# Kernel optimization log

Measured on AMD Instinct MI355X. Metric: run time of the kernel, lower is better.

## Reference

```python
import jax, jax.numpy as jnp
import numpy as np

B, T, D, H = 4, 1024, 512, 8
DK = D // H
P = 2 * T - 1  # relative position length


def rel_shift(x):
    # x: (b, h, t, 2t-1) -> (b, h, t, t), Transformer-XL relative shift
    b, h, t, p = x.shape
    x = jnp.pad(x, ((0, 0), (0, 0), (0, 0), (1, 0)))  # (b,h,t,p+1)
    x = x.reshape(b, h, p + 1, t)[:, :, 1:, :].reshape(b, h, t, p)
    return x[..., :t]


def setup_inputs() -> dict:
    key = jax.random.key(0)
    ks = jax.random.split(key, 16)
    s = 0.02
    return {
        "q": jax.random.normal(ks[0], (B, T, D), jnp.float32),
        "k": jax.random.normal(ks[1], (B, T, D), jnp.float32),
        "v": jax.random.normal(ks[2], (B, T, D), jnp.float32),
        "pos_emb": jax.random.normal(ks[3], (1, P, D), jnp.float32),
        "Wq": jax.random.normal(ks[4], (D, D), jnp.float32) * s,
        "bq": jnp.zeros((D,), jnp.float32),
        "Wk": jax.random.normal(ks[5], (D, D), jnp.float32) * s,
        "bk": jnp.zeros((D,), jnp.float32),
        "Wv": jax.random.normal(ks[6], (D, D), jnp.float32) * s,
        "bv": jnp.zeros((D,), jnp.float32),
        "Wp": jax.random.normal(ks[7], (D, D), jnp.float32) * s,
        "pos_bias_u": jax.random.normal(ks[8], (H, DK), jnp.float32) * s,
        "pos_bias_v": jax.random.normal(ks[9], (H, DK), jnp.float32) * s,
        "Wo": jax.random.normal(ks[10], (D, D), jnp.float32) * s,
        "bo": jnp.zeros((D,), jnp.float32),
    }


def reference(q, k, v, pos_emb, Wq, bq, Wk, bk, Wv, bv, Wp,
              pos_bias_u, pos_bias_v, Wo, bo):
    b, t, d = q.shape
    # QKV projections, split heads -> (b, t, h, dk)
    qh = (q @ Wq.T + bq).reshape(b, t, H, DK)
    kh = (k @ Wk.T + bk).reshape(b, t, H, DK)
    vh = (v @ Wv.T + bv).reshape(b, t, H, DK)
    # positional projection (no bias): (1, P, h, dk)
    ph = (pos_emb @ Wp.T).reshape(pos_emb.shape[1], H, DK)
    # content term: (q + u) . k
    q_u = qh + pos_bias_u  # (b,t,h,dk)
    matrix_ac = jnp.einsum("bqhd,bkhd->bhqk", q_u, kh)
    # position term: (q + v) . p, then relative shift
    q_v = qh + pos_bias_v
    matrix_bd = jnp.einsum("bqhd,phd->bhqp", q_v, ph)
    matrix_bd = rel_shift(matrix_bd)  # (b,h,t,t)
    scores = (matrix_ac + matrix_bd) / jnp.sqrt(jnp.float32(DK))
    attn = jax.nn.softmax(scores, axis=-1)
    out = jnp.einsum("bhqk,bkhd->bqhd", attn, vh).reshape(b, t, d)
    return out @ Wo.T + bo
```

## Files before the change

kernel.cpp:

```cpp
#include <hip/hip_runtime.h>
#include <math.h>

typedef unsigned short u16;
typedef _Float16 f16;
typedef __attribute__((ext_vector_type(8))) _Float16 f16x8;
typedef __attribute__((ext_vector_type(4))) float f32x4;

#define B_  4
#define T_  1024
#define D_  512
#define H_  8
#define DK_ 64
#define P_  2047

#define MFMAH(a, b, c) __builtin_amdgcn_mfma_f32_16x16x32_f16(a, b, c, 0, 0, 0)

__device__ __forceinline__ u16 f2hbits(float x) {
    union { f16 h; u16 u; } cv; cv.h = (f16)x; return cv.u;
}

__device__ __forceinline__ void gload_lds16(const u16* g, u16* l) {
    __builtin_amdgcn_global_load_lds(
        (const __attribute__((address_space(1))) void*)g,
        (__attribute__((address_space(3))) void*)l, 16, 0, 0);
}

__device__ __forceinline__ int swz8(int row, int colbase) {
    return row * 64 + (((colbase >> 3) ^ (row & 7)) << 3);
}

__global__ __launch_bounds__(256)
void conv_all(const float* __restrict__ q, const float* __restrict__ k,
              const float* __restrict__ v, const float* __restrict__ pe,
              const float* __restrict__ wq, const float* __restrict__ wk,
              const float* __restrict__ wv, const float* __restrict__ wp,
              const float* __restrict__ wo,
              u16* qs, u16* ks, u16* vs, u16* pes,
              u16* wqs, u16* wks, u16* wvs, u16* wps, u16* wos)
{
    const int NQ = 524288;
    const int NPE = 262016;
    const int NW = 65536;
    const int TOT = 3 * NQ + NPE + 5 * NW;
    for (int i = blockIdx.x * 256 + threadIdx.x; i < TOT; i += gridDim.x * 256) {
        const float* src; u16* dst; int off;
        int j = i;
        if (j < NQ)              { src = q;  dst = qs;  off = j; }
        else if ((j -= NQ) < NQ) { src = k;  dst = ks;  off = j; }
        else if ((j -= NQ) < NQ) { src = v;  dst = vs;  off = j; }
        else if ((j -= NQ) < NPE){ src = pe; dst = pes; off = j; }
        else if ((j -= NPE) < NW){ src = wq; dst = wqs; off = j; }
        else if ((j -= NW) < NW) { src = wk; dst = wks; off = j; }
        else if ((j -= NW) < NW) { src = wv; dst = wvs; off = j; }
        else if ((j -= NW) < NW) { src = wp; dst = wps; off = j; }
        else                     { j -= NW; src = wo; dst = wos; off = j; }
        float4 x = *(const float4*)(src + (size_t)off * 4);
        union { f16 h[4]; uint2 u2; } cv;
        cv.h[0] = (f16)x.x; cv.h[1] = (f16)x.y;
        cv.h[2] = (f16)x.z; cv.h[3] = (f16)x.w;
        *(uint2*)(dst + (size_t)off * 4) = cv.u2;
    }
}

__device__ __forceinline__ void gemm_core(
    const u16* __restrict__ A, const u16* __restrict__ Bw,
    int bm, int bn, int M, f32x4 (&acc)[4][4],
    u16 (&sA)[2][128][64], u16 (&sB)[2][128][64])
{
    const int tid = threadIdx.x;
    const int ln = tid & 63, w = tid >> 6;
    const int arow = ln & 15, kseg = ln >> 4;
    const int wr = w >> 1, wc = w & 1;

    auto stage = [&](int k0, int buf) {
        #pragma unroll
        for (int it = 0; it < 4; ++it) {
            int ch = it * 256 + tid;
            int r = ch >> 3, j = ch & 7;
            int rm = bm + r; if (rm > M - 1) rm = M - 1;
            gload_lds16(A + (size_t)rm * 512 + k0 + ((j ^ (r & 7)) << 3),
                        &sA[buf][0][0] + ch * 8);
        }
        #pragma unroll
        for (int it = 0; it < 4; ++it) {
            int ch = it * 256 + tid;
            int r = ch >> 3, j = ch & 7;
            gload_lds16(Bw + (size_t)(bn + r) * 512 + k0 + ((j ^ (r & 7)) << 3),
                        &sB[buf][0][0] + ch * 8);
        }
    };

    stage(0, 0);
    for (int t = 0; t < 8; ++t) {
        const int cur = t & 1;
        if (t < 7) {
            stage((t + 1) * 64, cur ^ 1);
            asm volatile("s_waitcnt vmcnt(8)" ::: "memory");
        } else {
            asm volatile("s_waitcnt vmcnt(0)" ::: "memory");
        }
        __builtin_amdgcn_sched_barrier(0);
        __builtin_amdgcn_s_barrier();

        f16x8 af[4][2], bf[4][2];
        #pragma unroll
        for (int mi = 0; mi < 4; ++mi) {
            int row = wr * 64 + mi * 16 + arow;
            #pragma unroll
            for (int kc = 0; kc < 2; ++kc)
                af[mi][kc] = *(const f16x8*)
                    (&sA[cur][row][0] + ((((kc << 2) | kseg) ^ (row & 7)) << 3));
        }
        #pragma unroll
        for (int nj = 0; nj < 4; ++nj) {
            int row = wc * 64 + nj * 16 + arow;
            #pragma unroll
            for (int kc = 0; kc < 2; ++kc)
                bf[nj][kc] = *(const f16x8*)
                    (&sB[cur][row][0] + ((((kc << 2) | kseg) ^ (row & 7)) << 3));
        }
        __builtin_amdgcn_s_setprio(1);
        #pragma unroll
        for (int mi = 0; mi < 4; ++mi)
            #pragma unroll
            for (int nj = 0; nj < 4; ++nj)
                #pragma unroll
                for (int kc = 0; kc < 2; ++kc)
                    acc[mi][nj] = MFMAH(af[mi][kc], bf[nj][kc], acc[mi][nj]);
        __builtin_amdgcn_s_setprio(0);

        asm volatile("" ::: "memory");
        __builtin_amdgcn_s_barrier();
        asm volatile("" ::: "memory");
    }
}

__global__ __launch_bounds__(256, 2)
void gemm_qkvp(const u16* __restrict__ qs, const u16* __restrict__ ks,
               const u16* __restrict__ vs, const u16* __restrict__ pes,
               const u16* __restrict__ wqs, const u16* __restrict__ wks,
               const u16* __restrict__ wvs, const u16* __restrict__ wps,
               const float* __restrict__ bq, const float* __restrict__ bk,
               const float* __restrict__ bv,
               const float* __restrict__ pbu, const float* __restrict__ pbv,
               u16* __restrict__ qub, u16* __restrict__ qvb,
               u16* __restrict__ kh, u16* __restrict__ vt, u16* __restrict__ ph)
{
    __shared__ u16 sA[2][128][64];
    __shared__ u16 sB[2][128][64];

    const int by = blockIdx.y;
    const u16 *A, *Bw; const float* bias;
    int seg, bm, M, Tn;
    if (by < 32)      { seg=0; bm=by*128;       A=qs;  Bw=wqs; bias=bq;      M=4096; Tn=T_; }
    else if (by < 64) { seg=1; bm=(by-32)*128;  A=ks;  Bw=wks; bias=bk;      M=4096; Tn=T_; }
    else if (by < 96) { seg=2; bm=(by-64)*128;  A=vs;  Bw=wvs; bias=bv;      M=4096; Tn=T_; }
    else              { seg=3; bm=(by-96)*128;  A=pes; Bw=wps; bias=nullptr; M=P_;   Tn=P_; }
    const int bn = blockIdx.x * 128;

    f32x4 acc[4][4] = {};
    gemm_core(A, Bw, bm, bn, M, acc, sA, sB);

    const int tid = threadIdx.x;
    const int ln = tid & 63, w = tid >> 6;
    const int arow = ln & 15, kseg = ln >> 4;
    const int wr = w >> 1, wc = w & 1;

    float bv0[4];
    #pragma unroll
    for (int nj = 0; nj < 4; ++nj)
        bv0[nj] = bias ? bias[bn + wc * 64 + nj * 16 + arow] : 0.f;

    #pragma unroll
    for (int mi = 0; mi < 4; ++mi)
        #pragma unroll
        for (int r = 0; r < 4; ++r) {
            int m = bm + wr * 64 + mi * 16 + kseg * 4 + r;
            if (m >= M) continue;
            #pragma unroll
            for (int nj = 0; nj < 4; ++nj) {
                int n = bn + wc * 64 + nj * 16 + arow;
                float val = acc[mi][nj][r] + bv0[nj];
                if (seg == 0) {
                    int bb = m >> 10, t = m & 1023;
                    int hh = n >> 6, d = n & 63;
                    size_t off = ((size_t)(bb * H_ + hh) * T_ + t) * 64 + d;
                    qub[off] = f2hbits((val + pbu[hh * 64 + d]) * 0.125f);
                    qvb[off] = f2hbits((val + pbv[hh * 64 + d]) * 0.125f);
                } else if (seg == 2) {
                    int bb = m >> 10, t = m & 1023;
                    int hh = n >> 6, d = n & 63;
                    vt[((size_t)(bb * H_ + hh) * 64 + d) * T_ + t] = f2hbits(val);
                } else {
                    int bb = (Tn == T_) ? (m >> 10) : 0;
                    int t = m - bb * Tn;
                    int hh = n >> 6, d = n & 63;
                    size_t off = ((size_t)(bb * H_ + hh) * Tn + t) * 64 + d;
                    if (seg == 1) kh[off] = f2hbits(val);
                    else          ph[off] = f2hbits(val);
                }
            }
        }
}

__global__ __launch_bounds__(256, 2)
void gemm_out(const u16* __restrict__ A, const u16* __restrict__ Bw,
              const float* __restrict__ bias, float* __restrict__ C)
{
    __shared__ u16 sA[2][128][64];
    __shared__ u16 sB[2][128][64];
    const int bn = blockIdx.x * 128;
    const int bm = blockIdx.y * 128;
    f32x4 acc[4][4] = {};
    gemm_core(A, Bw, bm, bn, 4096, acc, sA, sB);

    const int tid = threadIdx.x;
    const int ln = tid & 63, w = tid >> 6;
    const int arow = ln & 15, kseg = ln >> 4;
    const int wr = w >> 1, wc = w & 1;
    #pragma unroll
    for (int mi = 0; mi < 4; ++mi)
        #pragma unroll
        for (int r = 0; r < 4; ++r) {
            int m = bm + wr * 64 + mi * 16 + kseg * 4 + r;
            #pragma unroll
            for (int nj = 0; nj < 4; ++nj) {
                int n = bn + wc * 64 + nj * 16 + arow;
                C[(size_t)m * 512 + n] = acc[mi][nj][r] + bias[n];
            }
        }
}

__global__ __launch_bounds__(256, 2)
void relattn_mfma(const u16* __restrict__ qub, const u16* __restrict__ qvb,
                  const u16* __restrict__ kh, const u16* __restrict__ vt,
                  const u16* __restrict__ ph,
                  u16* __restrict__ ao)
{
    __shared__ u16 s_k[3][64][64];
    __shared__ u16 s_p[3][64][64];
    __shared__ u16 s_pp[4][16][64];

    const int tid = threadIdx.x;
    const int ln  = tid & 63;
    const int w   = tid >> 6;
    const int arow = ln & 15;
    const int kseg = ln >> 4;

    const int lg = ((blockIdx.x & 7) << 6) | (blockIdx.x >> 3);
    const int qt = lg & 15, h = (lg >> 4) & 7, b = lg >> 7;
    const int q0 = qt * 64;

    const size_t kvbase = (size_t)(b * H_ + h) * T_ * 64;
    const size_t vtbase = (size_t)(b * H_ + h) * 64 * T_;
    const size_t pbase  = (size_t)h * P_ * 64;
    const int jb0 = 960 - q0;

    f16x8 qu[2], qv[2];
    {
        const u16* qb = qub + kvbase + (size_t)(q0 + w * 16 + arow) * 64;
        const u16* vb = qvb + kvbase + (size_t)(q0 + w * 16 + arow) * 64;
        #pragma unroll
        for (int c = 0; c < 2; ++c) {
            qu[c] = *(const f16x8*)(qb + c * 32 + kseg * 8);
            qv[c] = *(const f16x8*)(vb + c * 32 + kseg * 8);
        }
    }

    f32x4 o_[4] = {};
    float l_run[4] = {};

    auto stage_k = [&](int kt, int slot) {
        #pragma unroll
        for (int it = 0; it < 2; ++it) {
            int idx = tid + it * 256;
            int r = idx >> 3, ch = idx & 7;
            const u16* src = kh + kvbase + (size_t)(kt * 64 + r) * 64 + ((ch ^ (r & 7)) << 3);
            gload_lds16(src, &s_k[slot][0][0] + idx * 8);
        }
    };
    auto stage_p = [&](int c, int slot) {
        #pragma unroll
        for (int it = 0; it < 2; ++it) {
            int idx = tid + it * 256;
            int r = idx >> 3, ch = idx & 7;
            int j = jb0 + c * 64 + r; if (j > P_ - 1) j = P_ - 1;
            const u16* src = ph + pbase + (size_t)j * 64 + ((ch ^ (r & 7)) << 3);
            gload_lds16(src, &s_p[slot][0][0] + idx * 8);
        }
    };
    auto bd_chunk = [&](int slot, f32x4* out) {
        #pragma unroll
        for (int nb = 0; nb < 4; ++nb) {
            int pr = nb * 16 + arow;
            f16x8 b0 = *(const f16x8*)(&s_p[slot][0][0] + swz8(pr, kseg * 8));
            f16x8 b1 = *(const f16x8*)(&s_p[slot][0][0] + swz8(pr, 32 + kseg * 8));
            out[nb] = MFMAH(qv[0], b0, out[nb]);
            out[nb] = MFMAH(qv[1], b1, out[nb]);
        }
    };

    stage_k(0, 0); stage_k(1, 1);
    stage_p(0, 0); stage_p(1, 1); stage_p(2, 2);
    __syncthreads();
    f32x4 carry[4] = {};
    bd_chunk(0, carry);
    asm volatile("" ::: "memory");
    __builtin_amdgcn_s_barrier();
    asm volatile("" ::: "memory");

    int ks = 0;
    for (int t = 0; t < 16; ++t) {
        const int k0 = t * 64;
        const int pr = (ks + 1 > 2) ? 0 : ks + 1;
        const int kw = (ks + 2 > 2) ? ks - 1 : ks + 2;

        f16x8 vfr[4][2];
        #pragma unroll
        for (int nt = 0; nt < 4; ++nt) {
            const u16* vp = vt + vtbase + (size_t)(nt * 16 + arow) * T_ + k0 + kseg * 8;
            vfr[nt][0] = *(const f16x8*)vp;
            vfr[nt][1] = *(const f16x8*)(vp + 32);
        }

        if (t < 14) { stage_k(t + 2, kw); stage_p(t + 3, ks); }

        __builtin_amdgcn_s_setprio(1);
        f32x4 ac[4] = {};
        #pragma unroll
        for (int nt = 0; nt < 4; ++nt) {
            int kr = nt * 16 + arow;
            f16x8 b0 = *(const f16x8*)(&s_k[ks][0][0] + swz8(kr, kseg * 8));
            f16x8 b1 = *(const f16x8*)(&s_k[ks][0][0] + swz8(kr, 32 + kseg * 8));
            ac[nt] = MFMAH(qu[0], b0, ac[nt]);
            ac[nt] = MFMAH(qu[1], b1, ac[nt]);
        }
        f32x4 bdn[4] = {};
        bd_chunk(pr, bdn);
        __builtin_amdgcn_s_setprio(0);

        float win[5][4];
        #pragma unroll
        for (int r = 0; r < 4; ++r) {
            if (w == 0)      { win[0][r]=carry[3][r]; win[1][r]=bdn[0][r];   win[2][r]=bdn[1][r];   win[3][r]=bdn[2][r];   win[4][r]=bdn[3][r]; }
            else if (w == 1) { win[0][r]=carry[2][r]; win[1][r]=carry[3][r]; win[2][r]=bdn[0][r];   win[3][r]=bdn[1][r];   win[4][r]=bdn[2][r]; }
            else if (w == 2) { win[0][r]=carry[1][r]; win[1][r]=carry[2][r]; win[2][r]=carry[3][r]; win[3][r]=bdn[0][r];   win[4][r]=bdn[1][r]; }
            else             { win[0][r]=carry[0][r]; win[1][r]=carry[1][r]; win[2][r]=carry[2][r]; win[3][r]=carry[3][r]; win[4][r]=bdn[0][r]; }
        }

        #pragma unroll
        for (int r = 0; r < 4; ++r) {
            int sl  = 15 - (kseg << 2) - r;
            int src = (ln & 48) | ((arow + sl) & 15);
            bool hi = (arow < sl);
            int r16 = kseg * 4 + r;
            #pragma unroll
            for (int nt = 0; nt < 4; ++nt) {
                float sel = hi ? win[nt + 1][r] : win[nt][r];
                float pm = __shfl(sel, src, 64);
                float pv = __expf(ac[nt][r] + pm);
                l_run[r] += pv;
                int kl = nt * 16 + arow;
                s_pp[w][r16][(((kl >> 3) ^ (r16 & 7)) << 3) | (kl & 7)] = f2hbits(pv);
            }
        }
        asm volatile("s_waitcnt lgkmcnt(0)" ::: "memory");
        __builtin_amdgcn_sched_barrier(0);

        f16x8 pa0 = *(const f16x8*)(&s_pp[w][arow][0] + ((kseg ^ (arow & 7)) << 3));
        f16x8 pa1 = *(const f16x8*)(&s_pp[w][arow][0] + (((4 + kseg) ^ (arow & 7)) << 3));
        __builtin_amdgcn_s_setprio(1);
        #pragma unroll
        for (int nt = 0; nt < 4; ++nt) {
            o_[nt] = MFMAH(pa0, vfr[nt][0], o_[nt]);
            o_[nt] = MFMAH(pa1, vfr[nt][1], o_[nt]);
        }
        __builtin_amdgcn_s_setprio(0);

        #pragma unroll
        for (int nb = 0; nb < 4; ++nb) carry[nb] = bdn[nb];

        asm volatile("" ::: "memory");
        __builtin_amdgcn_s_barrier();
        asm volatile("" ::: "memory");
        ks = pr;
    }

    #pragma unroll
    for (int r = 0; r < 4; ++r) {
        float l = l_run[r];
        l += __shfl_xor(l, 1); l += __shfl_xor(l, 2);
        l += __shfl_xor(l, 4); l += __shfl_xor(l, 8);
        l_run[r] = 1.f / l;
    }
    #pragma unroll
    for (int nt = 0; nt < 4; ++nt)
        #pragma unroll
        for (int r = 0; r < 4; ++r) {
            int qrow = q0 + w * 16 + kseg * 4 + r;
            size_t off = ((size_t)(b * T_ + qrow)) * D_ + h * DK_ + nt * 16 + arow;
            ao[off] = f2hbits(o_[nt][r] * l_run[r]);
        }
}

extern "C" void kernel_launch(void* const* d_in, const int* in_sizes, int n_in,
                              void* d_out, int out_size, void* d_ws, size_t ws_size,
                              hipStream_t stream)
{
    const float* q   = (const float*)d_in[0];
    const float* k   = (const float*)d_in[1];
    const float* v   = (const float*)d_in[2];
    const float* pe  = (const float*)d_in[3];
    const float* Wq  = (const float*)d_in[4];
    const float* bq  = (const float*)d_in[5];
    const float* Wk  = (const float*)d_in[6];
    const float* bk  = (const float*)d_in[7];
    const float* Wv  = (const float*)d_in[8];
    const float* bv  = (const float*)d_in[9];
    const float* Wp  = (const float*)d_in[10];
    const float* pbu = (const float*)d_in[11];
    const float* pbv = (const float*)d_in[12];
    const float* Wo  = (const float*)d_in[13];
    const float* bo  = (const float*)d_in[14];
    float* out = (float*)d_out;

    char* ws = (char*)d_ws;
    const size_t MB = 1024 * 1024;
    const size_t HMB = 512 * 1024;
    u16* qs  = (u16*)(ws);
    u16* ks  = (u16*)(ws + 4 * MB);
    u16* vs  = (u16*)(ws + 8 * MB);
    u16* pes = (u16*)(ws + 12 * MB);
    u16* wqs = (u16*)(ws + 17 * MB);
    u16* wks = (u16*)(ws + 17 * MB + HMB);
    u16* wvs = (u16*)(ws + 18 * MB);
    u16* wps = (u16*)(ws + 18 * MB + HMB);
    u16* wos = (u16*)(ws + 19 * MB);
    u16* qub = (u16*)(ws + 20 * MB);
    u16* qvb = (u16*)(ws + 24 * MB);
    u16* kh  = (u16*)(ws + 28 * MB);
    u16* vt  = (u16*)(ws + 32 * MB);
    u16* ph  = (u16*)(ws + 36 * MB);
    u16* ao  = (u16*)(ws + 38 * MB + HMB);

    dim3 blk(256);
    conv_all<<<dim3(2048), blk, 0, stream>>>(q, k, v, pe, Wq, Wk, Wv, Wp, Wo,
        qs, ks, vs, pes, wqs, wks, wvs, wps, wos);

    gemm_qkvp<<<dim3(4, 112), blk, 0, stream>>>(
        qs, ks, vs, pes, wqs, wks, wvs, wps,
        bq, bk, bv, pbu, pbv, qub, qvb, kh, vt, ph);

    relattn_mfma<<<dim3(512), blk, 0, stream>>>(qub, qvb, kh, vt, ph, ao);

    gemm_out<<<dim3(4, 32), blk, 0, stream>>>(ao, wos, bo, out);
}
```

Measured before the change: 86.44 us.

## Split attention key range into halves with 128-row query tiles and combine pass

The attention kernel now uses 512-thread blocks covering 128 query rows, and each block processes only half of the key sequence (split-K). It writes unnormalized fp32 partial outputs and row sums to workspace, and a new combine kernel adds the two halves and normalizes. This aims to raise per-block reuse of the staged K/P tiles and give each block a shorter serial loop. In exchange it adds an extra kernel launch and fp32 partial-result traffic, and the partial buffer reuses workspace regions that earlier kernels wrote.

```diff
diff --git a/kernel.cpp b/kernel.cpp
--- a/kernel.cpp
+++ b/kernel.cpp
@@ -231,15 +231,15 @@
         }
 }
 
-__global__ __launch_bounds__(256, 2)
+__global__ __launch_bounds__(512, 2)
 void relattn_mfma(const u16* __restrict__ qub, const u16* __restrict__ qvb,
                   const u16* __restrict__ kh, const u16* __restrict__ vt,
                   const u16* __restrict__ ph,
-                  u16* __restrict__ ao)
+                  float* __restrict__ po, float* __restrict__ lsum)
 {
     __shared__ u16 s_k[3][64][64];
     __shared__ u16 s_p[3][64][64];
-    __shared__ u16 s_pp[4][16][64];
+    __shared__ u16 s_pp[8][16][64];
 
     const int tid = threadIdx.x;
     const int ln  = tid & 63;
@@ -248,13 +248,15 @@
     const int kseg = ln >> 4;
 
     const int lg = ((blockIdx.x & 7) << 6) | (blockIdx.x >> 3);
-    const int qt = lg & 15, h = (lg >> 4) & 7, b = lg >> 7;
-    const int q0 = qt * 64;
+    const int qt = lg & 7, h = (lg >> 3) & 7, b = (lg >> 6) & 3;
+    const int half = lg >> 8;
+    const int q0 = qt * 128;
+    const int kbase = half * 512;
 
     const size_t kvbase = (size_t)(b * H_ + h) * T_ * 64;
     const size_t vtbase = (size_t)(b * H_ + h) * 64 * T_;
     const size_t pbase  = (size_t)h * P_ * 64;
-    const int jb0 = 960 - q0;
+    const int jb0 = 896 + kbase - q0;
 
     f16x8 qu[2], qv[2];
     {
@@ -271,30 +273,22 @@
     float l_run[4] = {};
 
     auto stage_k = [&](int kt, int slot) {
-        #pragma unroll
-        for (int it = 0; it < 2; ++it) {
-            int idx = tid + it * 256;
-            int r = idx >> 3, ch = idx & 7;
-            const u16* src = kh + kvbase + (size_t)(kt * 64 + r) * 64 + ((ch ^ (r & 7)) << 3);
-            gload_lds16(src, &s_k[slot][0][0] + idx * 8);
-        }
+        int r = tid >> 3, ch = tid & 7;
+        const u16* src = kh + kvbase + (size_t)(kbase + kt * 64 + r) * 64 + ((ch ^ (r & 7)) << 3);
+        gload_lds16(src, &s_k[slot][0][0] + tid * 8);
     };
     auto stage_p = [&](int c, int slot) {
-        #pragma unroll
-        for (int it = 0; it < 2; ++it) {
-            int idx = tid + it * 256;
-            int r = idx >> 3, ch = idx & 7;
-            int j = jb0 + c * 64 + r; if (j > P_ - 1) j = P_ - 1;
-            const u16* src = ph + pbase + (size_t)j * 64 + ((ch ^ (r & 7)) << 3);
-            gload_lds16(src, &s_p[slot][0][0] + idx * 8);
-        }
+        int r = tid >> 3, ch = tid & 7;
+        int j = jb0 + c * 64 + r; if (j > P_ - 1) j = P_ - 1;
+        const u16* src = ph + pbase + (size_t)j * 64 + ((ch ^ (r & 7)) << 3);
+        gload_lds16(src, &s_p[slot][0][0] + tid * 8);
     };
     auto bd_chunk = [&](int slot, f32x4* out) {
         #pragma unroll
         for (int nb = 0; nb < 4; ++nb) {
-            int pr = nb * 16 + arow;
-            f16x8 b0 = *(const f16x8*)(&s_p[slot][0][0] + swz8(pr, kseg * 8));
-            f16x8 b1 = *(const f16x8*)(&s_p[slot][0][0] + swz8(pr, 32 + kseg * 8));
+            int prr = nb * 16 + arow;
+            f16x8 b0 = *(const f16x8*)(&s_p[slot][0][0] + swz8(prr, kseg * 8));
+            f16x8 b1 = *(const f16x8*)(&s_p[slot][0][0] + swz8(prr, 32 + kseg * 8));
             out[nb] = MFMAH(qv[0], b0, out[nb]);
             out[nb] = MFMAH(qv[1], b1, out[nb]);
         }
@@ -303,16 +297,17 @@
     stage_k(0, 0); stage_k(1, 1);
     stage_p(0, 0); stage_p(1, 1); stage_p(2, 2);
     __syncthreads();
-    f32x4 carry[4] = {};
-    bd_chunk(0, carry);
+    f32x4 c2[4] = {}, c1[4] = {};
+    bd_chunk(0, c2);
+    bd_chunk(1, c1);
     asm volatile("" ::: "memory");
     __builtin_amdgcn_s_barrier();
     asm volatile("" ::: "memory");
+    stage_p(3, 0);
 
     int ks = 0;
-    for (int t = 0; t < 16; ++t) {
-        const int k0 = t * 64;
-        const int pr = (ks + 1 > 2) ? 0 : ks + 1;
+    for (int t = 0; t < 8; ++t) {
+        const int k0 = kbase + t * 64;
         const int kw = (ks + 2 > 2) ? ks - 1 : ks + 2;
 
         f16x8 vfr[4][2];
@@ -323,7 +318,10 @@
             vfr[nt][1] = *(const f16x8*)(vp + 32);
         }
 
-        if (t < 14) { stage_k(t + 2, kw); stage_p(t + 3, ks); }
+        if (t < 6) {
+            stage_k(t + 2, kw);
+            stage_p(t + 4, (ks + 1 > 2) ? 0 : ks + 1);
+        }
 
         __builtin_amdgcn_s_setprio(1);
         f32x4 ac[4] = {};
@@ -336,16 +334,22 @@
             ac[nt] = MFMAH(qu[1], b1, ac[nt]);
         }
         f32x4 bdn[4] = {};
-        bd_chunk(pr, bdn);
+        bd_chunk(kw, bdn);
         __builtin_amdgcn_s_setprio(0);
 
         float win[5][4];
         #pragma unroll
         for (int r = 0; r < 4; ++r) {
-            if (w == 0)      { win[0][r]=carry[3][r]; win[1][r]=bdn[0][r];   win[2][r]=bdn[1][r];   win[3][r]=bdn[2][r];   win[4][r]=bdn[3][r]; }
-            else if (w == 1) { win[0][r]=carry[2][r]; win[1][r]=carry[3][r]; win[2][r]=bdn[0][r];   win[3][r]=bdn[1][r];   win[4][r]=bdn[2][r]; }
-            else if (w == 2) { win[0][r]=carry[1][r]; win[1][r]=carry[2][r]; win[2][r]=carry[3][r]; win[3][r]=bdn[0][r];   win[4][r]=bdn[1][r]; }
-            else             { win[0][r]=carry[0][r]; win[1][r]=carry[1][r]; win[2][r]=carry[2][r]; win[3][r]=carry[3][r]; win[4][r]=bdn[0][r]; }
+            switch (w) {
+            case 7: win[0][r]=c2[0][r]; win[1][r]=c2[1][r]; win[2][r]=c2[2][r]; win[3][r]=c2[3][r]; win[4][r]=c1[0][r]; break;
+            case 6: win[0][r]=c2[1][r]; win[1][r]=c2[2][r]; win[2][r]=c2[3][r]; win[3][r]=c1[0][r]; win[4][r]=c1[1][r]; break;
+            case 5: win[0][r]=c2[2][r]; win[1][r]=c2[3][r]; win[2][r]=c1[0][r]; win[3][r]=c1[1][r]; win[4][r]=c1[2][r]; break;
+            case 4: win[0][r]=c2[3][r]; win[1][r]=c1[0][r]; win[2][r]=c1[1][r]; win[3][r]=c1[2][r]; win[4][r]=c1[3][r]; break;
+            case 3: win[0][r]=c1[0][r]; win[1][r]=c1[1][r]; win[2][r]=c1[2][r]; win[3][r]=c1[3][r]; win[4][r]=bdn[0][r]; break;
+            case 2: win[0][r]=c1[1][r]; win[1][r]=c1[2][r]; win[2][r]=c1[3][r]; win[3][r]=bdn[0][r]; win[4][r]=bdn[1][r]; break;
+            case 1: win[0][r]=c1[2][r]; win[1][r]=c1[3][r]; win[2][r]=bdn[0][r]; win[3][r]=bdn[1][r]; win[4][r]=bdn[2][r]; break;
+            default:win[0][r]=c1[3][r]; win[1][r]=bdn[0][r]; win[2][r]=bdn[1][r]; win[3][r]=bdn[2][r]; win[4][r]=bdn[3][r]; break;
+            }
         }
 
         #pragma unroll
@@ -378,12 +382,12 @@
         __builtin_amdgcn_s_setprio(0);
 
         #pragma unroll
-        for (int nb = 0; nb < 4; ++nb) carry[nb] = bdn[nb];
+        for (int nb = 0; nb < 4; ++nb) { c2[nb] = c1[nb]; c1[nb] = bdn[nb]; }
 
         asm volatile("" ::: "memory");
         __builtin_amdgcn_s_barrier();
         asm volatile("" ::: "memory");
-        ks = pr;
+        ks = (ks + 1 > 2) ? 0 : ks + 1;
     }
 
     #pragma unroll
@@ -391,16 +395,41 @@
         float l = l_run[r];
         l += __shfl_xor(l, 1); l += __shfl_xor(l, 2);
         l += __shfl_xor(l, 4); l += __shfl_xor(l, 8);
-        l_run[r] = 1.f / l;
-    }
+        l_run[r] = l;
+    }
+    float* poH = po + (size_t)half * 4096 * 512;
     #pragma unroll
     for (int nt = 0; nt < 4; ++nt)
         #pragma unroll
         for (int r = 0; r < 4; ++r) {
             int qrow = q0 + w * 16 + kseg * 4 + r;
-            size_t off = ((size_t)(b * T_ + qrow)) * D_ + h * DK_ + nt * 16 + arow;
-            ao[off] = f2hbits(o_[nt][r] * l_run[r]);
-        }
+            poH[(size_t)(b * T_ + qrow) * 512 + h * 64 + nt * 16 + arow] = o_[nt][r];
+        }
+    if (arow == 0) {
+        #pragma unroll
+        for (int r = 0; r < 4; ++r) {
+            int qrow = q0 + w * 16 + kseg * 4 + r;
+            lsum[(size_t)half * 32768 + (size_t)(b * T_ + qrow) * 8 + h] = l_run[r];
+        }
+    }
+}
+
+__global__ __launch_bounds__(256)
+void combine_halves(const float4* __restrict__ po0, const float4* __restrict__ po1,
+                    const float* __restrict__ l0, const float* __restrict__ l1,
+                    u16* __restrict__ ao)
+{
+    int i = blockIdx.x * 256 + threadIdx.x;
+    int row = i >> 7;
+    int h = (i >> 4) & 7;
+    float4 o1 = po0[i], o2 = po1[i];
+    float inv = 1.f / (l0[row * 8 + h] + l1[row * 8 + h]);
+    ushort4 r;
+    r.x = f2hbits((o1.x + o2.x) * inv);
+    r.y = f2hbits((o1.y + o2.y) * inv);
+    r.z = f2hbits((o1.z + o2.z) * inv);
+    r.w = f2hbits((o1.w + o2.w) * inv);
+    *(ushort4*)(ao + (size_t)i * 4) = r;
 }
 
 extern "C" void kernel_launch(void* const* d_in, const int* in_sizes, int n_in,
@@ -441,6 +470,8 @@
     u16* kh  = (u16*)(ws + 28 * MB);
     u16* vt  = (u16*)(ws + 32 * MB);
     u16* ph  = (u16*)(ws + 36 * MB);
+    float* po   = (float*)(ws);
+    float* lsum = (float*)(ws + 16 * MB);
     u16* ao  = (u16*)(ws + 38 * MB + HMB);
 
     dim3 blk(256);
@@ -451,7 +482,12 @@
         qs, ks, vs, pes, wqs, wks, wvs, wps,
         bq, bk, bv, pbu, pbv, qub, qvb, kh, vt, ph);
 
-    relattn_mfma<<<dim3(512), blk, 0, stream>>>(qub, qvb, kh, vt, ph, ao);
+    relattn_mfma<<<dim3(512), dim3(512), 0, stream>>>(qub, qvb, kh, vt, ph,
+                                                      po, lsum);
+
+    combine_halves<<<dim3(2048), blk, 0, stream>>>(
+        (const float4*)po, (const float4*)(po + (size_t)4096 * 512),
+        lsum, lsum + 32768, ao);
 
     gemm_out<<<dim3(4, 32), blk, 0, stream>>>(ao, wos, bo, out);
 }
```

Measured after the change: 121.3 us. 40.3% more time.
